# Kernel tuning notes

Hardware: AMD Instinct MI355X
Metric: run time of the kernel (lower is better)

## Reference

```python
import jax, jax.numpy as jnp
import numpy as np

B, N, D = 4, 2048, 1024
H = 16
HD = D // H


def setup_inputs() -> dict:
    key = jax.random.key(0)
    ks = jax.random.split(key, 6)
    x = jax.random.normal(ks[0], (B, N, D), dtype=jnp.float32)
    # additive causal mask: 0 on/below diagonal, -inf above
    neg = jnp.float32(-1e9)
    causal_mask = jnp.where(jnp.triu(jnp.ones((N, N), dtype=bool), k=1), neg, 0.0).astype(jnp.float32)
    s = 1.0 / np.sqrt(D)
    Wqkv = jax.random.normal(ks[1], (D, 3 * D), dtype=jnp.float32) * s
    bqkv = jax.random.normal(ks[2], (3 * D,), dtype=jnp.float32) * 0.01
    Wproj = jax.random.normal(ks[3], (D, D), dtype=jnp.float32) * s
    bproj = jax.random.normal(ks[4], (D,), dtype=jnp.float32) * 0.01
    return {"x": x, "causal_mask": causal_mask, "Wqkv": Wqkv, "bqkv": bqkv, "Wproj": Wproj, "bproj": bproj}


def reference(x, causal_mask, Wqkv, bqkv, Wproj, bproj):
    b, n, d = x.shape
    qkv = x @ Wqkv + bqkv  # [B,N,3D]
    qkv = qkv.reshape(b, n, 3, H, HD).transpose(2, 0, 3, 1, 4)  # [3,B,H,N,HD]
    q, k, v = qkv[0], qkv[1], qkv[2]
    scale = HD ** -0.5
    attn = jnp.einsum('bhqd,bhkd->bhqk', q, k) * scale  # [B,H,N,N]
    attn = attn + causal_mask  # broadcast [N,N] -> [B,H,N,N]
    attn = jax.nn.softmax(attn, axis=-1)
    out = jnp.einsum('bhqk,bhkd->bhqd', attn, v)  # [B,H,N,HD]
    out = out.transpose(0, 2, 1, 3).reshape(b, n, d)
    return out @ Wproj + bproj
```

## Files before the change

kernel.cpp:

```cpp
#include <hip/hip_runtime.h>
#include <hip/hip_bf16.h>

typedef unsigned short u16;
typedef unsigned int u32;
typedef __attribute__((ext_vector_type(8))) short bf16x8;
typedef __attribute__((ext_vector_type(4))) float f32x4;
typedef __attribute__((ext_vector_type(16))) float f32x16;

#define AS1(p) ((const __attribute__((address_space(1))) void*)(p))
#define AS3(p) ((__attribute__((address_space(3))) void*)(p))
#define STG(src, dst) __builtin_amdgcn_global_load_lds(AS1(src), AS3(dst), 16, 0, 0)

#if __has_builtin(__builtin_amdgcn_exp2f)
#define EXP2F(x) __builtin_amdgcn_exp2f(x)
#else
#define EXP2F(x) exp2f(x)
#endif

#define VT_BH_STRIDE 131072

static __device__ __forceinline__ float b2f(u16 u) {
  union { unsigned int i; float f; } v; v.i = ((unsigned int)u) << 16; return v.f;
}
static __device__ __forceinline__ u16 f2b(float f) {
  union { float f; unsigned int i; } v; v.f = f;
  unsigned int r = v.i + 0x7FFFu + ((v.i >> 16) & 1u);
  return (u16)(r >> 16);
}
static __device__ __forceinline__ u32 cvt_pk_bf16(float lo, float hi) {
  u32 r;
  asm("v_cvt_pk_bf16_f32 %0, %1, %2" : "=v"(r) : "v"(lo), "v"(hi));
  return r;
}
static __device__ __forceinline__ void permswap(u32& a, u32& b) {
  asm("v_permlane32_swap_b32 %0, %1" : "+v"(a), "+v"(b));
}

__global__ __launch_bounds__(256) void prep(const float* __restrict__ x, u16* __restrict__ xb,
                                            const float* __restrict__ Wqkv, u16* __restrict__ wqkvT,
                                            const float* __restrict__ Wproj, u16* __restrict__ wprojT) {
  __shared__ float tile[32][33];
  const int bid = blockIdx.x, t = threadIdx.x;
  if (bid < 2048) {
    const int n8 = 8192 * 1024 / 8;
    for (int i = bid * 256 + t; i < n8; i += 2048 * 256) {
      const float4* s = (const float4*)(x + (size_t)i * 8);
      float4 a = s[0], b = s[1];
      bf16x8 o;
      o[0] = (short)f2b(a.x); o[1] = (short)f2b(a.y); o[2] = (short)f2b(a.z); o[3] = (short)f2b(a.w);
      o[4] = (short)f2b(b.x); o[5] = (short)f2b(b.y); o[6] = (short)f2b(b.z); o[7] = (short)f2b(b.w);
      *(bf16x8*)(xb + (size_t)i * 8) = o;
    }
  } else {
    const float* src; u16* dst; int R, C, cx, ry;
    if (bid < 5120) { const int l = bid - 2048; src = Wqkv; dst = wqkvT; R = 1024; C = 3072; cx = l % 96; ry = l / 96; }
    else            { const int l = bid - 5120; src = Wproj; dst = wprojT; R = 1024; C = 1024; cx = l & 31; ry = l >> 5; }
    const int c0 = cx * 32, r0 = ry * 32;
    const int tx = t & 31, ty = t >> 5;
    for (int i = ty; i < 32; i += 8) tile[i][tx] = src[(size_t)(r0 + i) * C + c0 + tx];
    __syncthreads();
    for (int i = ty; i < 32; i += 8) dst[(size_t)(c0 + i) * R + r0 + tx] = f2b(tile[tx][i]);
  }
}

template <typename OutT, bool WVT>
__global__ __launch_bounds__(256) void gemm_bt_bias(
    const u16* __restrict__ A,
    const u16* __restrict__ BT,
    const float* __restrict__ bias,
    OutT* __restrict__ C,
    int M, int N, int K,
    u16* __restrict__ vt) {
  __shared__ alignas(16) u16 Als[128 * 32];
  __shared__ alignas(16) u16 Bls[128 * 32];
  const int m0 = blockIdx.x * 128, n0 = blockIdx.y * 128;
  const int t = threadIdx.x;
  const int w = t >> 6, lane = t & 63;
  const int wr = w >> 1, wc = w & 1;
  const int rlo = lane & 15, g = lane >> 4;

  f32x4 acc[4][4] = {};

  const int r0 = t >> 2;
  const int c0 = (t & 3) << 3;
  const u16* aSrc = A + (size_t)(m0 + r0) * K + c0;
  const u16* bSrc = BT + (size_t)(n0 + r0) * K + c0;

  for (int k0 = 0; k0 < K; k0 += 32) {
    __builtin_amdgcn_global_load_lds(AS1(aSrc + k0), AS3(&Als[t * 8]), 16, 0, 0);
    __builtin_amdgcn_global_load_lds(AS1(aSrc + (size_t)64 * K + k0), AS3(&Als[(t + 256) * 8]), 16, 0, 0);
    __builtin_amdgcn_global_load_lds(AS1(bSrc + k0), AS3(&Bls[t * 8]), 16, 0, 0);
    __builtin_amdgcn_global_load_lds(AS1(bSrc + (size_t)64 * K + k0), AS3(&Bls[(t + 256) * 8]), 16, 0, 0);
    __syncthreads();

    bf16x8 a[4], b[4];
    #pragma unroll
    for (int m = 0; m < 4; ++m)
      a[m] = *(const bf16x8*)&Als[(wr * 64 + m * 16 + rlo) * 32 + g * 8];
    #pragma unroll
    for (int n = 0; n < 4; ++n)
      b[n] = *(const bf16x8*)&Bls[(wc * 64 + n * 16 + rlo) * 32 + g * 8];
    #pragma unroll
    for (int m = 0; m < 4; ++m)
      #pragma unroll
      for (int n = 0; n < 4; ++n)
        acc[m][n] = __builtin_amdgcn_mfma_f32_16x16x32_bf16(a[m], b[n], acc[m][n], 0, 0, 0);
    __syncthreads();
  }

  #pragma unroll
  for (int n = 0; n < 4; ++n) {
    const int col = n0 + wc * 64 + n * 16 + rlo;
    const float bv = bias[col];
    #pragma unroll
    for (int m = 0; m < 4; ++m) {
      const int row = m0 + wr * 64 + m * 16 + g * 4;
      u16 tmp[4];
      #pragma unroll
      for (int i = 0; i < 4; ++i) {
        float r = acc[m][n][i] + bv;
        if constexpr (sizeof(OutT) == 2) {
          const u16 hv = f2b(r);
          C[(size_t)(row + i) * N + col] = (OutT)hv;
          if constexpr (WVT) tmp[i] = hv;
        } else {
          C[(size_t)(row + i) * N + col] = (OutT)r;
        }
      }
      if constexpr (WVT) {
        if (col >= 2048) {
          const int cv = col - 2048;
          const int h = cv >> 6, dd = cv & 63;
          const int b = row >> 11, nloc = row & 2047;
          uint2 pv;
          pv.x = (u32)tmp[0] | ((u32)tmp[1] << 16);
          pv.y = (u32)tmp[2] | ((u32)tmp[3] << 16);
          *(uint2*)&vt[(size_t)(b * 16 + h) * VT_BH_STRIDE + (nloc >> 2) * 256 + dd * 4] = pv;
        }
      }
    }
  }
}

__global__ __launch_bounds__(256, 2) void attn_fwd(
    const u16* __restrict__ qkv,
    const u16* __restrict__ VT,
    u16* __restrict__ O) {
  const int N = 2048, TD = 3072, D = 1024;
  const int bid = blockIdx.x;
  const int qp = bid >> 6, bh = bid & 63;
  const int b = bh >> 4, h = bh & 15;
  const int t = threadIdx.x, w = t >> 6, lane = t & 63;
  const int l31 = lane & 31, hi = lane >> 5;
  const int qh = w >> 1, st = w & 1;

  __shared__ alignas(16) u16 pool16[2][2][64 * 64];
  __shared__ float rsLds[2][32];
  float* poolf = (float*)&pool16[0][0][0];

  const int c1 = t, c2 = t + 256;
  const int r1 = c1 >> 3, sc1 = ((c1 & 7) ^ (r1 & 7)) * 8;
  const int r2 = c2 >> 3, sc2 = ((c2 & 7) ^ (r2 & 7)) * 8;
  const u16* kbase = qkv + (size_t)(b * N) * TD + D + h * 64;
  const u16* vbase = VT + (size_t)bh * VT_BH_STRIDE;

#define ASTAGE(buf, j0) do { \
    STG(kbase + (size_t)((j0) + r1) * TD + sc1, &pool16[buf][0][c1 * 8]); \
    STG(kbase + (size_t)((j0) + r2) * TD + sc2, &pool16[buf][0][c2 * 8]); \
    STG(vbase + (size_t)(j0) * 64 + c1 * 8, &pool16[buf][1][c1 * 8]); \
    STG(vbase + (size_t)(j0) * 64 + c2 * 8, &pool16[buf][1][c2 * 8]); } while (0)

  const float L2E = 1.44269504089f;
  const float NSH = -23.0830992f;

  for (int pass = 0; pass < 2; ++pass) {
    const int qt = pass ? (15 - qp) : qp;
    const int qbw = qt * 128 + qh * 64;

    bf16x8 qf[2][4];
    #pragma unroll
    for (int qs = 0; qs < 2; ++qs) {
      const u16* qp_ = qkv + ((size_t)(b * N) + qbw + qs * 32 + l31) * TD + h * 64 + hi * 8;
      #pragma unroll
      for (int c = 0; c < 4; ++c) {
        bf16x8 v = *(const bf16x8*)(qp_ + c * 16);
        #pragma unroll
        for (int j = 0; j < 8; ++j)
          v[j] = (short)f2b(b2f((u16)v[j]) * 0.125f);
        qf[qs][c] = v;
      }
    }

    f32x16 o_acc[2][2] = {};
    float psum[2] = {0.f, 0.f};
    const int jend = qt * 128 + 64;

    ASTAGE(0, 0);
    __syncthreads();

    int cur = 0;
    for (int j0 = 0; j0 <= jend; j0 += 64) {
      if (j0 + 64 <= jend) ASTAGE(cur ^ 1, j0 + 64);

      const int sb2 = j0 + st * 32;
      if (sb2 <= qbw + 63) {
        bf16x8 kf[4];
        {
          const int row = st * 32 + l31, sw = (row & 7) << 3;
          #pragma unroll
          for (int c = 0; c < 4; ++c)
            kf[c] = *(const bf16x8*)&pool16[cur][0][row * 64 + ((c * 16 + hi * 8) ^ sw)];
        }
        bf16x8 vf[2][2];
        #pragma unroll
        for (int dt = 0; dt < 2; ++dt) {
          const int dd = dt * 32 + l31;
          #pragma unroll
          for (int kc = 0; kc < 2; ++kc) {
            const int nb = st * 32 + kc * 16 + hi * 8;
            union { uint2 q[2]; bf16x8 v; } u;
            u.q[0] = *(const uint2*)&pool16[cur][1][(nb >> 2) * 256 + dd * 4];
            u.q[1] = *(const uint2*)&pool16[cur][1][(nb >> 2) * 256 + 256 + dd * 4];
            vf[kc][dt] = u.v;
          }
        }

        #pragma unroll
        for (int qs = 0; qs < 2; ++qs) {
          if (qs == 0 && sb2 > qbw + 31) continue;
          const int qr = qbw + qs * 32 + l31;
          f32x16 S = {};
          __builtin_amdgcn_s_setprio(1);
          #pragma unroll
          for (int c = 0; c < 4; ++c)
            S = __builtin_amdgcn_mfma_f32_32x32x16_bf16(kf[c], qf[qs][c], S, 0, 0, 0);
          __builtin_amdgcn_s_setprio(0);
          if (sb2 + 31 > qbw + qs * 32) {
            const int kvb = sb2 + 4 * hi;
            #pragma unroll
            for (int r = 0; r < 16; ++r)
              if (kvb + (r & 3) + 8 * (r >> 2) > qr) S[r] = -1e30f;
          }
          float p[16];
          #pragma unroll
          for (int r = 0; r < 16; ++r) p[r] = EXP2F(fmaf(S[r], L2E, NSH));
          float ps = 0.f;
          #pragma unroll
          for (int r = 0; r < 16; ++r) ps += p[r];
          psum[qs] += ps;
          u32 wq[8];
          #pragma unroll
          for (int i = 0; i < 8; ++i) wq[i] = cvt_pk_bf16(p[2 * i], p[2 * i + 1]);
          permswap(wq[0], wq[2]); permswap(wq[1], wq[3]);
          permswap(wq[4], wq[6]); permswap(wq[5], wq[7]);
          union { u32 u[4]; bf16x8 v; } pa0, pa1;
          pa0.u[0] = wq[0]; pa0.u[1] = wq[1]; pa0.u[2] = wq[2]; pa0.u[3] = wq[3];
          pa1.u[0] = wq[4]; pa1.u[1] = wq[5]; pa1.u[2] = wq[6]; pa1.u[3] = wq[7];
          __builtin_amdgcn_s_setprio(1);
          #pragma unroll
          for (int dt = 0; dt < 2; ++dt) {
            o_acc[qs][dt] = __builtin_amdgcn_mfma_f32_32x32x16_bf16(pa0.v, vf[0][dt], o_acc[qs][dt], 0, 0, 0);
            o_acc[qs][dt] = __builtin_amdgcn_mfma_f32_32x32x16_bf16(pa1.v, vf[1][dt], o_acc[qs][dt], 0, 0, 0);
          }
          __builtin_amdgcn_s_setprio(0);
        }
      }
      __syncthreads();
      cur ^= 1;
    }

    float rsown[2];
    #pragma unroll
    for (int qs = 0; qs < 2; ++qs)
      rsown[qs] = psum[qs] + __shfl_xor(psum[qs], 32, 64);

    #pragma unroll
    for (int qs = 0; qs < 2; ++qs) {
      if (st != qs) {
        #pragma unroll
        for (int dt = 0; dt < 2; ++dt)
          #pragma unroll
          for (int r = 0; r < 16; ++r)
            poolf[qh * 2048 + (dt * 16 + r) * 64 + lane] = o_acc[qs][dt][r];
        rsLds[qh][l31] = rsown[qs];
      }
      __syncthreads();
      if (st == qs) {
        const float inv = 1.0f / (rsown[qs] + rsLds[qh][l31]);
        #pragma unroll
        for (int r = 0; r < 16; ++r) {
          const int qrow = (r & 3) + 8 * (r >> 2) + 4 * hi;
          const float invq = __shfl(inv, qrow, 64);
          const int q = qbw + qs * 32 + qrow;
          #pragma unroll
          for (int dt = 0; dt < 2; ++dt) {
            const float val = o_acc[qs][dt][r] + poolf[qh * 2048 + (dt * 16 + r) * 64 + lane];
            O[((size_t)(b * N) + q) * D + h * 64 + dt * 32 + l31] = f2b(val * invq);
          }
        }
      }
      __syncthreads();
    }
  }
#undef ASTAGE
}

extern "C" void kernel_launch(void* const* d_in, const int* in_sizes, int n_in,
                              void* d_out, int out_size, void* d_ws, size_t ws_size,
                              hipStream_t stream) {
  const float* x     = (const float*)d_in[0];
  const float* Wqkv  = (const float*)d_in[2];
  const float* bqkv  = (const float*)d_in[3];
  const float* Wproj = (const float*)d_in[4];
  const float* bproj = (const float*)d_in[5];
  float* out = (float*)d_out;

  const int B = 4, N = 2048, D = 1024, H = 16;
  const int BN = B * N;
  const int TD = 3 * D;

  char* ws = (char*)d_ws;
  u16* qkv    = (u16*)(ws);
  u16* vt     = (u16*)(ws + 50331648);
  u16* aout   = (u16*)(ws + 67108864);
  u16* wqkvT  = (u16*)(ws + 83886080);
  u16* wprojT = (u16*)(ws + 90177536);
  u16* xb     = (u16*)(ws + 92274688);

  prep<<<6144, 256, 0, stream>>>(x, xb, Wqkv, wqkvT, Wproj, wprojT);
  gemm_bt_bias<u16, true><<<dim3(BN / 128, TD / 128), 256, 0, stream>>>(xb, wqkvT, bqkv, qkv, BN, TD, D, vt);
  attn_fwd<<<512, 256, 0, stream>>>(qkv, vt, aout);
  gemm_bt_bias<float, false><<<dim3(BN / 128, D / 128), 256, 0, stream>>>(aout, wprojT, bproj, out, BN, D, D, nullptr);
}
```

Baseline: 179.2 us.

## Halve attention query tile to 64 rows and double grid for occupancy

Each attention block now covers 64 query rows (32 per wave pair) instead of 128, and the grid doubles to 1024 blocks. Each wave keeps one Q fragment set and one accumulator pair, which cuts register use enough to raise launch bounds to 4 blocks per CU. Causal load balancing still pairs tile qp with tile 31-qp. In exchange, each staged K/V tile is reused by half as many queries, so global and LDS traffic for K/V per unit of work roughly doubles.

```diff
diff --git a/kernel.cpp b/kernel.cpp
--- a/kernel.cpp
+++ b/kernel.cpp
@@ -142,7 +142,7 @@
   }
 }
 
-__global__ __launch_bounds__(256, 2) void attn_fwd(
+__global__ __launch_bounds__(256, 4) void attn_fwd(
     const u16* __restrict__ qkv,
     const u16* __restrict__ VT,
     u16* __restrict__ O) {
@@ -174,26 +174,25 @@
   const float NSH = -23.0830992f;
 
   for (int pass = 0; pass < 2; ++pass) {
-    const int qt = pass ? (15 - qp) : qp;
-    const int qbw = qt * 128 + qh * 64;
-
-    bf16x8 qf[2][4];
-    #pragma unroll
-    for (int qs = 0; qs < 2; ++qs) {
-      const u16* qp_ = qkv + ((size_t)(b * N) + qbw + qs * 32 + l31) * TD + h * 64 + hi * 8;
+    const int qt = pass ? (31 - qp) : qp;
+    const int qbw = qt * 64 + qh * 32;
+
+    bf16x8 qf[4];
+    {
+      const u16* qp_ = qkv + ((size_t)(b * N) + qbw + l31) * TD + h * 64 + hi * 8;
       #pragma unroll
       for (int c = 0; c < 4; ++c) {
         bf16x8 v = *(const bf16x8*)(qp_ + c * 16);
         #pragma unroll
         for (int j = 0; j < 8; ++j)
           v[j] = (short)f2b(b2f((u16)v[j]) * 0.125f);
-        qf[qs][c] = v;
-      }
-    }
-
-    f32x16 o_acc[2][2] = {};
-    float psum[2] = {0.f, 0.f};
-    const int jend = qt * 128 + 64;
+        qf[c] = v;
+      }
+    }
+
+    f32x16 o_acc[2] = {};
+    float psum = 0.f;
+    const int jend = qt * 64;
 
     ASTAGE(0, 0);
     __syncthreads();
@@ -203,7 +202,7 @@
       if (j0 + 64 <= jend) ASTAGE(cur ^ 1, j0 + 64);
 
       const int sb2 = j0 + st * 32;
-      if (sb2 <= qbw + 63) {
+      if (sb2 <= qbw + 31) {
         bf16x8 kf[4];
         {
           const int row = st * 32 + l31, sw = (row & 7) << 3;
@@ -225,82 +224,71 @@
           }
         }
 
-        #pragma unroll
-        for (int qs = 0; qs < 2; ++qs) {
-          if (qs == 0 && sb2 > qbw + 31) continue;
-          const int qr = qbw + qs * 32 + l31;
-          f32x16 S = {};
-          __builtin_amdgcn_s_setprio(1);
+        const int qr = qbw + l31;
+        f32x16 S = {};
+        __builtin_amdgcn_s_setprio(1);
+        #pragma unroll
+        for (int c = 0; c < 4; ++c)
+          S = __builtin_amdgcn_mfma_f32_32x32x16_bf16(kf[c], qf[c], S, 0, 0, 0);
+        __builtin_amdgcn_s_setprio(0);
+        if (sb2 + 31 > qbw) {
+          const int kvb = sb2 + 4 * hi;
           #pragma unroll
-          for (int c = 0; c < 4; ++c)
-            S = __builtin_amdgcn_mfma_f32_32x32x16_bf16(kf[c], qf[qs][c], S, 0, 0, 0);
-          __builtin_amdgcn_s_setprio(0);
-          if (sb2 + 31 > qbw + qs * 32) {
-            const int kvb = sb2 + 4 * hi;
-            #pragma unroll
-            for (int r = 0; r < 16; ++r)
-              if (kvb + (r & 3) + 8 * (r >> 2) > qr) S[r] = -1e30f;
-          }
-          float p[16];
-          #pragma unroll
-          for (int r = 0; r < 16; ++r) p[r] = EXP2F(fmaf(S[r], L2E, NSH));
-          float ps = 0.f;
-          #pragma unroll
-          for (int r = 0; r < 16; ++r) ps += p[r];
-          psum[qs] += ps;
-          u32 wq[8];
-          #pragma unroll
-          for (int i = 0; i < 8; ++i) wq[i] = cvt_pk_bf16(p[2 * i], p[2 * i + 1]);
-          permswap(wq[0], wq[2]); permswap(wq[1], wq[3]);
-          permswap(wq[4], wq[6]); permswap(wq[5], wq[7]);
-          union { u32 u[4]; bf16x8 v; } pa0, pa1;
-          pa0.u[0] = wq[0]; pa0.u[1] = wq[1]; pa0.u[2] = wq[2]; pa0.u[3] = wq[3];
-          pa1.u[0] = wq[4]; pa1.u[1] = wq[5]; pa1.u[2] = wq[6]; pa1.u[3] = wq[7];
-          __builtin_amdgcn_s_setprio(1);
-          #pragma unroll
-          for (int dt = 0; dt < 2; ++dt) {
-            o_acc[qs][dt] = __builtin_amdgcn_mfma_f32_32x32x16_bf16(pa0.v, vf[0][dt], o_acc[qs][dt], 0, 0, 0);
-            o_acc[qs][dt] = __builtin_amdgcn_mfma_f32_32x32x16_bf16(pa1.v, vf[1][dt], o_acc[qs][dt], 0, 0, 0);
-          }
-          __builtin_amdgcn_s_setprio(0);
-        }
+          for (int r = 0; r < 16; ++r)
+            if (kvb + (r & 3) + 8 * (r >> 2) > qr) S[r] = -1e30f;
+        }
+        float p[16];
+        #pragma unroll
+        for (int r = 0; r < 16; ++r) p[r] = EXP2F(fmaf(S[r], L2E, NSH));
+        float ps = 0.f;
+        #pragma unroll
+        for (int r = 0; r < 16; ++r) ps += p[r];
+        psum += ps;
+        u32 wq[8];
+        #pragma unroll
+        for (int i = 0; i < 8; ++i) wq[i] = cvt_pk_bf16(p[2 * i], p[2 * i + 1]);
+        permswap(wq[0], wq[2]); permswap(wq[1], wq[3]);
+        permswap(wq[4], wq[6]); permswap(wq[5], wq[7]);
+        union { u32 u[4]; bf16x8 v; } pa0, pa1;
+        pa0.u[0] = wq[0]; pa0.u[1] = wq[1]; pa0.u[2] = wq[2]; pa0.u[3] = wq[3];
+        pa1.u[0] = wq[4]; pa1.u[1] = wq[5]; pa1.u[2] = wq[6]; pa1.u[3] = wq[7];
+        __builtin_amdgcn_s_setprio(1);
+        #pragma unroll
+        for (int dt = 0; dt < 2; ++dt) {
+          o_acc[dt] = __builtin_amdgcn_mfma_f32_32x32x16_bf16(pa0.v, vf[0][dt], o_acc[dt], 0, 0, 0);
+          o_acc[dt] = __builtin_amdgcn_mfma_f32_32x32x16_bf16(pa1.v, vf[1][dt], o_acc[dt], 0, 0, 0);
+        }
+        __builtin_amdgcn_s_setprio(0);
       }
       __syncthreads();
       cur ^= 1;
     }
 
-    float rsown[2];
-    #pragma unroll
-    for (int qs = 0; qs < 2; ++qs)
-      rsown[qs] = psum[qs] + __shfl_xor(psum[qs], 32, 64);
-
-    #pragma unroll
-    for (int qs = 0; qs < 2; ++qs) {
-      if (st != qs) {
-        #pragma unroll
-        for (int dt = 0; dt < 2; ++dt)
-          #pragma unroll
-          for (int r = 0; r < 16; ++r)
-            poolf[qh * 2048 + (dt * 16 + r) * 64 + lane] = o_acc[qs][dt][r];
-        rsLds[qh][l31] = rsown[qs];
-      }
-      __syncthreads();
-      if (st == qs) {
-        const float inv = 1.0f / (rsown[qs] + rsLds[qh][l31]);
-        #pragma unroll
-        for (int r = 0; r < 16; ++r) {
-          const int qrow = (r & 3) + 8 * (r >> 2) + 4 * hi;
-          const float invq = __shfl(inv, qrow, 64);
-          const int q = qbw + qs * 32 + qrow;
-          #pragma unroll
-          for (int dt = 0; dt < 2; ++dt) {
-            const float val = o_acc[qs][dt][r] + poolf[qh * 2048 + (dt * 16 + r) * 64 + lane];
-            O[((size_t)(b * N) + q) * D + h * 64 + dt * 32 + l31] = f2b(val * invq);
-          }
-        }
-      }
-      __syncthreads();
-    }
+    float rsown = psum + __shfl_xor(psum, 32, 64);
+    if (st == 1) {
+      #pragma unroll
+      for (int dt = 0; dt < 2; ++dt)
+        #pragma unroll
+        for (int r = 0; r < 16; ++r)
+          poolf[qh * 2048 + (dt * 16 + r) * 64 + lane] = o_acc[dt][r];
+      rsLds[qh][l31] = rsown;
+    }
+    __syncthreads();
+    if (st == 0) {
+      const float inv = 1.0f / (rsown + rsLds[qh][l31]);
+      #pragma unroll
+      for (int r = 0; r < 16; ++r) {
+        const int qrow = (r & 3) + 8 * (r >> 2) + 4 * hi;
+        const float invq = __shfl(inv, qrow, 64);
+        const int q = qbw + qrow;
+        #pragma unroll
+        for (int dt = 0; dt < 2; ++dt) {
+          const float val = o_acc[dt][r] + poolf[qh * 2048 + (dt * 16 + r) * 64 + lane];
+          O[((size_t)(b * N) + q) * D + h * 64 + dt * 32 + l31] = f2b(val * invq);
+        }
+      }
+    }
+    __syncthreads();
   }
 #undef ASTAGE
 }
@@ -329,6 +317,6 @@
 
   prep<<<6144, 256, 0, stream>>>(x, xb, Wqkv, wqkvT, Wproj, wprojT);
   gemm_bt_bias<u16, true><<<dim3(BN / 128, TD / 128), 256, 0, stream>>>(xb, wqkvT, bqkv, qkv, BN, TD, D, vt);
-  attn_fwd<<<512, 256, 0, stream>>>(qkv, vt, aout);
+  attn_fwd<<<1024, 256, 0, stream>>>(qkv, vt, aout);
   gemm_bt_bias<float, false><<<dim3(BN / 128, D / 128), 256, 0, stream>>>(aout, wprojT, bproj, out, BN, D, D, nullptr);
 }
```

Measured after the change: 183.1 us. 1.02x slower.

## Replace QKV GEMM with 256x256-tile 8-wave pipelined kernel

Applied to the files above, without the earlier changes.

Adds a new QKV projection GEMM that uses 256x256 output tiles, 512 threads and 64-wide K steps. A/B tiles are double-buffered in LDS through global_load_lds, with an XOR swizzle against bank conflicts, and the MFMA phases are interleaved with prefetches under explicit barriers and vmcnt waits. The launch order is swizzled across groups of 8 blocks for cache locality. The larger tiles raise data reuse per loaded byte and overlap loads with compute, at the cost of occupancy (one block per CU, large LDS use) and only 384 workgroups.

```diff
diff --git a/kernel.cpp b/kernel.cpp
--- a/kernel.cpp
+++ b/kernel.cpp
@@ -60,6 +60,142 @@
     for (int i = ty; i < 32; i += 8) tile[i][tx] = src[(size_t)(r0 + i) * C + c0 + tx];
     __syncthreads();
     for (int i = ty; i < 32; i += 8) dst[(size_t)(c0 + i) * R + r0 + tx] = f2b(tile[tx][i]);
+  }
+}
+
+template <bool WVT>
+__global__ __launch_bounds__(512, 1) void gemm8p(
+    const u16* __restrict__ A,
+    const u16* __restrict__ BT,
+    const float* __restrict__ bias,
+    u16* __restrict__ C,
+    int M, int N, int K, int nn,
+    u16* __restrict__ vt) {
+  __shared__ alignas(16) u16 As[2][2][128 * 64];
+  __shared__ alignas(16) u16 Bs[2][2][128 * 64];
+
+  const int nwg = gridDim.x, cpx = nwg >> 3, id0 = blockIdx.x;
+  const int swz = (id0 & 7) * cpx + (id0 >> 3);
+  const int mi = swz / nn, ni = swz % nn;
+  const int m0 = mi * 256, n0 = ni * 256;
+
+  const int t = threadIdx.x;
+  const int wid = t >> 6, lane = t & 63;
+  const int wr = wid >> 2, wc = wid & 3;
+  const int rlo = lane & 15, g = lane >> 4;
+
+  const int ca = t, cb = t + 512;
+  const int ra = ca >> 3, sca = ((ca & 7) ^ (ra & 7)) * 8;
+  const int rb = cb >> 3, scb = ((cb & 7) ^ (rb & 7)) * 8;
+  const u16* aP[2][2];
+  const u16* bP[2][2];
+  #pragma unroll
+  for (int h = 0; h < 2; ++h) {
+    aP[h][0] = A + (size_t)(m0 + h * 128 + ra) * K + sca;
+    aP[h][1] = A + (size_t)(m0 + h * 128 + rb) * K + scb;
+    bP[h][0] = BT + (size_t)(n0 + h * 128 + ra) * K + sca;
+    bP[h][1] = BT + (size_t)(n0 + h * 128 + rb) * K + scb;
+  }
+
+  f32x4 acc[8][4] = {};
+  bf16x8 a[4][2], b[2][2];
+  const int NT = K >> 6;
+
+#define BAR() __builtin_amdgcn_s_barrier()
+#define VM2() asm volatile("s_waitcnt vmcnt(2)" ::: "memory")
+#define VM0() asm volatile("s_waitcnt vmcnt(0)" ::: "memory")
+#define STAGE_A(h, jt) do { if ((jt) < NT) { const size_t ko_ = (size_t)(jt) * 64; \
+    STG(aP[h][0] + ko_, &As[(jt) & 1][h][t * 8]); \
+    STG(aP[h][1] + ko_, &As[(jt) & 1][h][(t + 512) * 8]); } } while (0)
+#define STAGE_B(h, jt) do { if ((jt) < NT) { const size_t ko_ = (size_t)(jt) * 64; \
+    STG(bP[h][0] + ko_, &Bs[(jt) & 1][h][t * 8]); \
+    STG(bP[h][1] + ko_, &Bs[(jt) & 1][h][(t + 512) * 8]); } } while (0)
+#define RDA(buf, mh) _Pragma("unroll") for (int fr = 0; fr < 4; ++fr) \
+    _Pragma("unroll") for (int kc = 0; kc < 2; ++kc) { \
+      const int r_ = (mh) * 64 + fr * 16 + rlo; \
+      a[fr][kc] = *(const bf16x8*)&As[buf][wr][r_ * 64 + ((kc * 32 + g * 8) ^ ((r_ & 7) << 3))]; }
+#define RDB(buf, nh) _Pragma("unroll") for (int fn = 0; fn < 2; ++fn) \
+    _Pragma("unroll") for (int kc = 0; kc < 2; ++kc) { \
+      const int r_ = (wc & 1) * 64 + (nh) * 32 + fn * 16 + rlo; \
+      b[fn][kc] = *(const bf16x8*)&Bs[buf][wc >> 1][r_ * 64 + ((kc * 32 + g * 8) ^ ((r_ & 7) << 3))]; }
+#define MM(mh, nh) __builtin_amdgcn_s_setprio(1); \
+    _Pragma("unroll") for (int fr = 0; fr < 4; ++fr) \
+      _Pragma("unroll") for (int fn = 0; fn < 2; ++fn) { \
+        f32x4 v_ = acc[(mh) * 4 + fr][(nh) * 2 + fn]; \
+        v_ = __builtin_amdgcn_mfma_f32_16x16x32_bf16(a[fr][0], b[fn][0], v_, 0, 0, 0); \
+        v_ = __builtin_amdgcn_mfma_f32_16x16x32_bf16(a[fr][1], b[fn][1], v_, 0, 0, 0); \
+        acc[(mh) * 4 + fr][(nh) * 2 + fn] = v_; } \
+    __builtin_amdgcn_s_setprio(0)
+
+  STAGE_A(0, 0); STAGE_A(1, 0); STAGE_B(0, 0); STAGE_B(1, 0); STAGE_A(0, 1);
+  VM2(); BAR();
+
+  const int NI = NT >> 1;
+  #pragma unroll 1
+  for (int it = 0; it < NI; ++it) {
+    const int kt1 = 2 * it + 1;
+    RDA(0, 0) RDB(0, 0)
+    STAGE_A(1, kt1);
+    BAR(); MM(0, 0); BAR();
+    RDB(0, 1)
+    STAGE_B(0, kt1);
+    BAR(); MM(0, 1); BAR();
+    RDA(0, 1)
+    STAGE_B(1, kt1);
+    BAR(); MM(1, 1); BAR();
+    RDB(0, 0)
+    STAGE_A(0, kt1 + 1);
+    if (kt1 + 1 < NT) { VM2(); } else { VM0(); }
+    BAR(); MM(1, 0); BAR();
+    RDA(1, 0) RDB(1, 0)
+    STAGE_A(1, kt1 + 1);
+    BAR(); MM(0, 0); BAR();
+    RDB(1, 1)
+    STAGE_B(0, kt1 + 1);
+    BAR(); MM(0, 1); BAR();
+    RDA(1, 1)
+    STAGE_B(1, kt1 + 1);
+    BAR(); MM(1, 1); BAR();
+    RDB(1, 0)
+    STAGE_A(0, kt1 + 2);
+    if (kt1 + 1 < NT) { if (kt1 + 2 < NT) { VM2(); } else { VM0(); } }
+    BAR(); MM(1, 0); BAR();
+  }
+#undef BAR
+#undef VM2
+#undef VM0
+#undef STAGE_A
+#undef STAGE_B
+#undef RDA
+#undef RDB
+#undef MM
+
+  #pragma unroll
+  for (int nr = 0; nr < 4; ++nr) {
+    const int col = n0 + wc * 64 + nr * 16 + rlo;
+    const float bv = bias[col];
+    #pragma unroll
+    for (int mr = 0; mr < 8; ++mr) {
+      const int row = m0 + wr * 128 + mr * 16 + g * 4;
+      u16 tmp[4];
+      #pragma unroll
+      for (int i = 0; i < 4; ++i) {
+        const u16 hv = f2b(acc[mr][nr][i] + bv);
+        C[(size_t)(row + i) * N + col] = hv;
+        tmp[i] = hv;
+      }
+      if constexpr (WVT) {
+        if (col >= 2048) {
+          const int cv = col - 2048;
+          const int h = cv >> 6, dd = cv & 63;
+          const int b = row >> 11, nloc = row & 2047;
+          uint2 pv;
+          pv.x = (u32)tmp[0] | ((u32)tmp[1] << 16);
+          pv.y = (u32)tmp[2] | ((u32)tmp[3] << 16);
+          *(uint2*)&vt[(size_t)(b * 16 + h) * VT_BH_STRIDE + (nloc >> 2) * 256 + dd * 4] = pv;
+        }
+      }
+    }
   }
 }
 
@@ -115,28 +251,13 @@
     #pragma unroll
     for (int m = 0; m < 4; ++m) {
       const int row = m0 + wr * 64 + m * 16 + g * 4;
-      u16 tmp[4];
       #pragma unroll
       for (int i = 0; i < 4; ++i) {
         float r = acc[m][n][i] + bv;
-        if constexpr (sizeof(OutT) == 2) {
-          const u16 hv = f2b(r);
-          C[(size_t)(row + i) * N + col] = (OutT)hv;
-          if constexpr (WVT) tmp[i] = hv;
-        } else {
+        if constexpr (sizeof(OutT) == 2)
+          C[(size_t)(row + i) * N + col] = (OutT)f2b(r);
+        else
           C[(size_t)(row + i) * N + col] = (OutT)r;
-        }
-      }
-      if constexpr (WVT) {
-        if (col >= 2048) {
-          const int cv = col - 2048;
-          const int h = cv >> 6, dd = cv & 63;
-          const int b = row >> 11, nloc = row & 2047;
-          uint2 pv;
-          pv.x = (u32)tmp[0] | ((u32)tmp[1] << 16);
-          pv.y = (u32)tmp[2] | ((u32)tmp[3] << 16);
-          *(uint2*)&vt[(size_t)(b * 16 + h) * VT_BH_STRIDE + (nloc >> 2) * 256 + dd * 4] = pv;
-        }
       }
     }
   }
@@ -328,7 +449,7 @@
   u16* xb     = (u16*)(ws + 92274688);
 
   prep<<<6144, 256, 0, stream>>>(x, xb, Wqkv, wqkvT, Wproj, wprojT);
-  gemm_bt_bias<u16, true><<<dim3(BN / 128, TD / 128), 256, 0, stream>>>(xb, wqkvT, bqkv, qkv, BN, TD, D, vt);
+  gemm8p<true><<<384, 512, 0, stream>>>(xb, wqkvT, bqkv, qkv, BN, TD, D, 12, vt);
   attn_fwd<<<512, 256, 0, stream>>>(qkv, vt, aout);
   gemm_bt_bias<float, false><<<dim3(BN / 128, D / 128), 256, 0, stream>>>(aout, wprojT, bproj, out, BN, D, D, nullptr);
 }
```

Result: no change. 178.0 us (-0.7%).
